# Performance work log

Hardware: AMD Instinct MI355X
Metric: run time of the kernel (lower is better)

The kernel has to match this reference:

```python
import jax, jax.numpy as jnp
import numpy as np

B, S, D = 32, 512, 512
H, DK, DV, DFF = 8, 64, 64, 2048
TEMP = float(np.sqrt(DK))  # d_k ** 0.5
COS_EPS = 1e-8             # torch.cosine_similarity eps
LN_EPS = 1e-5


def _layernorm(x, g, b):
    mu = jnp.mean(x, axis=-1, keepdims=True)
    var = jnp.var(x, axis=-1, keepdims=True)
    return (x - mu) * jax.lax.rsqrt(var + LN_EPS) * g + b


def setup_inputs() -> dict:
    key = jax.random.key(0)
    ks = jax.random.split(key, 12)
    s = 0.02
    return {
        "x": jax.random.normal(ks[0], (B, S, D), dtype=jnp.float32),
        "w_q": jax.random.normal(ks[1], (D, H * DK), dtype=jnp.float32) * s,
        "w_k": jax.random.normal(ks[2], (D, H * DK), dtype=jnp.float32) * s,
        "w_v": jax.random.normal(ks[3], (D, H * DV), dtype=jnp.float32) * s,
        "w_o": jax.random.normal(ks[4], (H * DV, D), dtype=jnp.float32) * s,
        "w_ff1": jax.random.normal(ks[5], (D, DFF), dtype=jnp.float32) * s,
        "b_ff1": jnp.zeros((DFF,), dtype=jnp.float32),
        "w_ff2": jax.random.normal(ks[6], (DFF, D), dtype=jnp.float32) * s,
        "b_ff2": jnp.zeros((D,), dtype=jnp.float32),
        "g1": jnp.ones((D,), dtype=jnp.float32),
        "b1": jnp.zeros((D,), dtype=jnp.float32),
        "g2": jnp.ones((D,), dtype=jnp.float32),
        "b2": jnp.zeros((D,), dtype=jnp.float32),
    }


def reference(x, w_q, w_k, w_v, w_o, w_ff1, b_ff1, w_ff2, b_ff2, g1, b1, g2, b2):
    b, s, _ = x.shape
    # projections -> [b, h, s, d]
    q = (x @ w_q).reshape(b, s, H, DK).transpose(0, 2, 1, 3)
    k = (x @ w_k).reshape(b, s, H, DK).transpose(0, 2, 1, 3)
    v = (x @ w_v).reshape(b, s, H, DV).transpose(0, 2, 1, 3)
    # cosine-similarity attention: dot(q,k) / max(||q||*||k||, eps) / temperature
    scores = jnp.einsum("bhqd,bhkd->bhqk", q, k)
    nq = jnp.linalg.norm(q, axis=-1)  # [b,h,s]
    nk = jnp.linalg.norm(k, axis=-1)
    denom = jnp.maximum(nq[:, :, :, None] * nk[:, :, None, :], COS_EPS)
    attn = jax.nn.softmax(scores / denom / TEMP, axis=-1)
    out = jnp.einsum("bhqk,bhkd->bhqd", attn, v)  # [b,h,s,dv]
    out = out.transpose(0, 2, 1, 3).reshape(b, s, H * DV) @ w_o
    # residual + LN1
    h1 = _layernorm(x + out, g1, b1)
    # FFN
    ffn = jax.nn.relu(h1 @ w_ff1 + b_ff1) @ w_ff2 + b_ff2
    # residual + LN2
    return _layernorm(h1 + ffn, g2, b2)
```

## Files before the change

kernel.cpp:

```cpp
#include <hip/hip_runtime.h>
#include <cmath>

typedef __bf16 bf16x8 __attribute__((ext_vector_type(8)));
typedef __bf16 bf16x4 __attribute__((ext_vector_type(4)));
typedef float  floatx4 __attribute__((ext_vector_type(4)));

#define LN_EPS 1e-5f
#define INV_TEMP 0.125f

static const int Mrows = 16384;

__device__ __forceinline__ void gload_lds16(const void* g, void* l) {
  __builtin_amdgcn_global_load_lds(
      (const __attribute__((address_space(1))) void*)g,
      (__attribute__((address_space(3))) void*)l, 16, 0, 0);
}

__global__ __launch_bounds__(256) void prep_kernel(const float* __restrict__ x, __bf16* __restrict__ xb,
                                                   const float* __restrict__ wq, const float* __restrict__ wk,
                                                   const float* __restrict__ wv, const float* __restrict__ wo,
                                                   const float* __restrict__ wff1, const float* __restrict__ wff2,
                                                   __bf16* __restrict__ tq, __bf16* __restrict__ tk,
                                                   __bf16* __restrict__ tv, __bf16* __restrict__ to_,
                                                   __bf16* __restrict__ tff1, __bf16* __restrict__ tff2) {
  const int bid = blockIdx.x, tid = threadIdx.x;
  if (bid < 8192) {
    int i = bid * 256 + tid;
    float4 v = ((const float4*)x)[i];
    __bf16* d = xb + i * 4;
    d[0] = (__bf16)v.x; d[1] = (__bf16)v.y; d[2] = (__bf16)v.z; d[3] = (__bf16)v.w;
    return;
  }
  __shared__ __bf16 til[64][72];
  int t = bid - 8192;
  const float* src; __bf16* dst; int R, C, bx, by;
  if (t < 256) {
    int w = t >> 6, tt = t & 63;
    const float* srcs[4] = {wq, wk, wv, wo};
    __bf16* dsts[4] = {tq, tk, tv, to_};
    src = srcs[w]; dst = dsts[w]; R = 512; C = 512; bx = tt & 7; by = tt >> 3;
  } else if (t < 512) {
    int tt = t - 256;
    src = wff1; dst = tff1; R = 512; C = 2048; bx = tt & 31; by = tt >> 5;
  } else {
    int tt = t - 512;
    src = wff2; dst = tff2; R = 2048; C = 512; bx = tt & 7; by = tt >> 3;
  }
  const float* s = src + (size_t)(by * 64) * C + bx * 64;
  int r = tid >> 4, c4 = (tid & 15) * 4;
  for (int p = 0; p < 4; ++p) {
    int rr = r + p * 16;
    float4 v = *(const float4*)(s + (size_t)rr * C + c4);
    til[c4 + 0][rr] = (__bf16)v.x;
    til[c4 + 1][rr] = (__bf16)v.y;
    til[c4 + 2][rr] = (__bf16)v.z;
    til[c4 + 3][rr] = (__bf16)v.w;
  }
  __syncthreads();
  __bf16* d = dst + (size_t)(bx * 64) * R + by * 64;
  int orow = tid >> 3, oc8 = (tid & 7) * 8;
  for (int p = 0; p < 2; ++p) {
    int rr = orow + p * 32;
    *(bf16x8*)(d + (size_t)rr * R + oc8) = *(const bf16x8*)(&til[rr][oc8]);
  }
}

template <int EPI, int NBN, int NDIM, int KDIM, int NKS>
__global__ __launch_bounds__(512, 4) void gemm256(const __bf16* __restrict__ A,
                                                  const __bf16* __restrict__ Bt,
                                                  __bf16* __restrict__ Cv,
                                                  const float* __restrict__ bias,
                                                  float* __restrict__ norms,
                                                  __bf16* __restrict__ vtg) {
  __shared__ __align__(16) char smem[73728];
  const int tid = threadIdx.x;
  const int wave = tid >> 6, lane = tid & 63;
  const int l15 = lane & 15, quad = lane >> 4;
  const int wm = wave >> 2, wn = wave & 3;

  constexpr int NBM = Mrows / 128;
  constexpr int NBLK = NBM * NBN * NKS;
  constexpr int KS = KDIM / NKS;
  constexpr int NTH = KS / 32;

  int id = blockIdx.x;
  int t = (id & 7) * (NBLK >> 3) + (id >> 3);
  const int ks = t / (NBM * NBN);
  t -= ks * (NBM * NBN);
  const int nblk = t % NBN, mblk = t / NBN;
  const int m0 = mblk * 128, n0 = nblk * 256;
  const __bf16* Ab = A + (size_t)ks * KS;
  const __bf16* Bb = Bt + (size_t)ks * KS;
  __bf16* Cw = Cv + (size_t)ks * Mrows * NDIM;
  (void)bias;

  const int l3 = lane >> 3, s_ = lane & 7;
  const int rl = l3 * 2 + (s_ >> 2);
  const int ksw = (s_ & 3) ^ (l3 & 3);
  const __bf16* sb[3];
  int ldo[3];
#pragma unroll
  for (int j = 0; j < 3; ++j) {
    int c = wave * 3 + j;
    int isB = c >= 8 ? 1 : 0;
    int cc = c - isB * 8;
    int row = cc * 16 + rl;
    sb[j] = (isB ? Bb + (size_t)(n0 + row) * KDIM
                 : Ab + (size_t)(m0 + row) * KDIM) + ksw * 8;
    ldo[j] = isB * 8192 + cc * 1024 + lane * 16;
  }

  const int lrt = (l15 >> 1) * 128 + (((l15 & 1) * 4 + (quad ^ ((l15 >> 1) & 3))) * 16);

  floatx4 zero = {0.f, 0.f, 0.f, 0.f};
  floatx4 acc[4][4];
#pragma unroll
  for (int i = 0; i < 4; ++i)
#pragma unroll
    for (int j = 0; j < 4; ++j) acc[i][j] = zero;

#define STAGEH(h, slotIdx)                                                   \
  {                                                                          \
    _Pragma("unroll") for (int j = 0; j < 3; ++j)                            \
        gload_lds16(sb[j] + (h) * 32, smem + (slotIdx) * 24576 + ldo[j]);    \
  }

#define READMFMA(slotIdx)                                                    \
  {                                                                          \
    const char* slotp = smem + (slotIdx) * 24576;                            \
    bf16x8 aF[4], bF[4];                                                     \
    _Pragma("unroll") for (int i = 0; i < 4; ++i)                            \
      aF[i] = *(const bf16x8*)(slotp + (wm * 4 + i) * 1024 + lrt);           \
    _Pragma("unroll") for (int j = 0; j < 4; ++j)                            \
      bF[j] = *(const bf16x8*)(slotp + 8192 + (wn * 4 + j) * 1024 + lrt);    \
    DOSTAGE_HOOK;                                                            \
    __builtin_amdgcn_s_setprio(1);                                           \
    _Pragma("unroll") for (int i = 0; i < 4; ++i)                            \
      _Pragma("unroll") for (int j = 0; j < 4; ++j)                          \
        acc[i][j] = __builtin_amdgcn_mfma_f32_16x16x32_bf16(aF[i], bF[j],    \
                                                            acc[i][j], 0, 0, 0); \
    __builtin_amdgcn_s_setprio(0);                                           \
  }

  STAGEH(0, 0);
  STAGEH(1, 1);

  int sl = 0;
  for (int h = 0; h < NTH - 1; ++h) {
    asm volatile("s_waitcnt vmcnt(3)" ::: "memory");
    __builtin_amdgcn_s_barrier();
    int st = (sl == 0) ? 2 : sl - 1;
    if (h < NTH - 2) {
#define DOSTAGE_HOOK STAGEH(h + 2, st)
      READMFMA(sl);
#undef DOSTAGE_HOOK
    } else {
#define DOSTAGE_HOOK
      READMFMA(sl);
#undef DOSTAGE_HOOK
    }
    sl = (sl == 2) ? 0 : sl + 1;
  }
  asm volatile("s_waitcnt vmcnt(0)" ::: "memory");
  __builtin_amdgcn_s_barrier();
#define DOSTAGE_HOOK
  READMFMA(sl);
#undef DOSTAGE_HOOK

#undef STAGEH
#undef READMFMA

  if (EPI == 4) {
    int head_global = (n0 + wn * 64) >> 6;
    int kind = head_global >> 3;
    if (kind < 2) {
      int h = head_global & 7;
#pragma unroll
      for (int ii = 0; ii < 4; ++ii)
#pragma unroll
        for (int r = 0; r < 4; ++r) {
          float sq = 0.f;
#pragma unroll
          for (int jj = 0; jj < 4; ++jj) {
            float v = acc[ii][jj][r];
            sq += v * v;
          }
          for (int m = 1; m < 16; m <<= 1) sq += __shfl_xor(sq, m, 64);
          if (l15 == 0) {
            int arow = m0 + wm * 64 + ii * 16 + quad * 4 + r;
            int bb = arow >> 9, ss = arow & 511;
            norms[kind * 131072 + ((bb << 3) + h) * 512 + ss] = rsqrtf(sq);
          }
        }
    } else {
      const int PADT = 72;
      __bf16* Ct = (__bf16*)smem;
      int bb = m0 >> 9, s0r = m0 & 511;
#pragma unroll
      for (int hh = 0; hh < 2; ++hh) {
        __builtin_amdgcn_s_barrier();
        if (wm == hh) {
#pragma unroll
          for (int ii = 0; ii < 4; ++ii)
#pragma unroll
            for (int jj = 0; jj < 4; ++jj) {
              bf16x4 pk;
#pragma unroll
              for (int r = 0; r < 4; ++r) pk[r] = (__bf16)acc[ii][jj][r];
              *(bf16x4*)(Ct + (wn * 64 + jj * 16 + l15) * PADT + ii * 16 + quad * 4) = pk;
            }
        }
        __builtin_amdgcn_s_barrier();
#pragma unroll
        for (int p = 0; p < 4; ++p) {
          int c = p * 64 + (tid >> 3);
          int s8 = (tid & 7) * 8;
          int h = ((n0 + c) >> 6) & 7, d = c & 63;
          *(bf16x8*)(vtg + ((size_t)(((bb << 3) + h) * 64 + d)) * 512 + s0r + hh * 64 + s8) =
              *(const bf16x8*)(Ct + c * PADT + s8);
        }
      }
      return;
    }
  }

  const int PADC = 264;
  __bf16* Cs = (__bf16*)smem;
  float bv[4];
  if (EPI == 2) {
#pragma unroll
    for (int j = 0; j < 4; ++j) bv[j] = bias[n0 + wn * 64 + j * 16 + l15];
  }
#pragma unroll
  for (int hh = 0; hh < 2; ++hh) {
    __builtin_amdgcn_s_barrier();
    if (wm == hh) {
#pragma unroll
      for (int i = 0; i < 4; ++i)
#pragma unroll
        for (int j = 0; j < 4; ++j)
#pragma unroll
          for (int r = 0; r < 4; ++r) {
            float v = acc[i][j][r];
            if (EPI == 2) {
              v += bv[j];
              v = v > 0.f ? v : 0.f;
            }
            Cs[(i * 16 + quad * 4 + r) * PADC + wn * 64 + j * 16 + l15] = (__bf16)v;
          }
    }
    __builtin_amdgcn_s_barrier();
#pragma unroll
    for (int p = 0; p < 4; ++p) {
      int rowl = p * 16 + (tid >> 5);
      int c8 = (tid & 31) * 8;
      *(bf16x8*)(Cw + (size_t)(m0 + hh * 64 + rowl) * NDIM + n0 + c8) =
          *(const bf16x8*)(Cs + rowl * PADC + c8);
    }
  }
}

__global__ __launch_bounds__(256) void attn_kernel(const __bf16* __restrict__ qkv,
                                                   const __bf16* __restrict__ vtg,
                                                   const float* __restrict__ norms,
                                                   __bf16* __restrict__ out) {
  __shared__ __align__(16) __bf16 KV[2][8192];
  __shared__ __align__(16) __bf16 P2[4][16 * 72];
  const int tid = threadIdx.x, wave = tid >> 6, lane = tid & 63;
  const int l15 = lane & 15, quad = lane >> 4;
  const int bh = blockIdx.x & 255;
  const int qq = blockIdx.x >> 8;
  const int b = bh >> 3, h = bh & 7;
  const int qbase = qq * 128 + wave * 32;
  const int rs = lane >> 3;
  const int swz_st = ((lane & 7) ^ rs) * 8;
  const int s7 = l15 & 7;

  const __bf16* Qb = qkv + (size_t)(b * 512) * 1536 + h * 64;
  const __bf16* Kb = Qb + 512;
  const __bf16* Vtb = vtg + (size_t)bh * 32768;
  const float* nkinv = norms + 131072 + bh * 512;
  const float* nqinv = norms + bh * 512;
  __bf16* Pw = P2[wave];

  bf16x8 aq[2][2];
  float cq[2];
  for (int ch = 0; ch < 2; ++ch) {
    int qrow = qbase + ch * 16;
    aq[ch][0] = *(const bf16x8*)(Qb + (size_t)(qrow + l15) * 1536 + quad * 8);
    aq[ch][1] = *(const bf16x8*)(Qb + (size_t)(qrow + l15) * 1536 + 32 + quad * 8);
    cq[ch] = nqinv[qrow + l15] * INV_TEMP;
  }

  floatx4 zero = {0.f, 0.f, 0.f, 0.f};
  floatx4 o[2][4];
  float lsum[2] = {0.f, 0.f};
  for (int ch = 0; ch < 2; ++ch)
    for (int jd = 0; jd < 4; ++jd) o[ch][jd] = zero;

#define STAGEKV(kt, s)                                                        \
  {                                                                           \
    int s0q = (kt) * 64;                                                      \
    _Pragma("unroll") for (int c = 0; c < 4; ++c) {                           \
      int g = wave * 4 + c;                                                   \
      const __bf16* src;                                                      \
      __bf16* dst;                                                            \
      if (g < 8) {                                                            \
        int sk = g * 8 + rs;                                                  \
        src = Kb + (size_t)(s0q + sk) * 1536 + swz_st;                        \
        dst = KV[s] + g * 512;                                                \
      } else {                                                                \
        int g2 = g - 8;                                                       \
        int dd = g2 * 8 + rs;                                                 \
        src = Vtb + (size_t)dd * 512 + s0q + swz_st;                          \
        dst = KV[s] + 4096 + g2 * 512;                                        \
      }                                                                       \
      gload_lds16(src, dst + lane * 8);                                       \
    }                                                                         \
  }

  STAGEKV(0, 0);

  for (int kt = 0; kt < 8; ++kt) {
    int s0 = kt * 64;
    int sl = kt & 1;
    asm volatile("s_waitcnt vmcnt(0)" ::: "memory");
    __builtin_amdgcn_s_barrier();
    if (kt < 7) STAGEKV(kt + 1, sl ^ 1);
    const __bf16* Ks = KV[sl];
    const __bf16* Vs = KV[sl] + 4096;

    floatx4 nk[4];
#pragma unroll
    for (int j = 0; j < 4; ++j)
      nk[j] = *(const floatx4*)(nkinv + s0 + j * 16 + quad * 4);

    bf16x8 kf[4][2];
#pragma unroll
    for (int j = 0; j < 4; ++j) {
      int r64 = (j * 16 + l15) * 64;
      kf[j][0] = *(const bf16x8*)(Ks + r64 + ((quad ^ s7) * 8));
      kf[j][1] = *(const bf16x8*)(Ks + r64 + (((4 + quad) ^ s7) * 8));
    }

    floatx4 z[2][4];
    __builtin_amdgcn_s_setprio(1);
#pragma unroll
    for (int ch = 0; ch < 2; ++ch)
#pragma unroll
      for (int j = 0; j < 4; ++j) {
        floatx4 zz = zero;
        zz = __builtin_amdgcn_mfma_f32_16x16x32_bf16(kf[j][0], aq[ch][0], zz, 0, 0, 0);
        zz = __builtin_amdgcn_mfma_f32_16x16x32_bf16(kf[j][1], aq[ch][1], zz, 0, 0, 0);
        z[ch][j] = zz;
      }
    __builtin_amdgcn_s_setprio(0);

    bf16x8 vf[4][2];
#pragma unroll
    for (int jd = 0; jd < 4; ++jd) {
      int r64 = (jd * 16 + l15) * 64;
      vf[jd][0] = *(const bf16x8*)(Vs + r64 + ((quad ^ s7) * 8));
      vf[jd][1] = *(const bf16x8*)(Vs + r64 + (((4 + quad) ^ s7) * 8));
    }

#pragma unroll
    for (int ch = 0; ch < 2; ++ch) {
#pragma unroll
      for (int j = 0; j < 4; ++j) {
        bf16x4 pk;
#pragma unroll
        for (int r = 0; r < 4; ++r) {
          float p = __expf(z[ch][j][r] * cq[ch] * nk[j][r]);
          lsum[ch] += p;
          pk[r] = (__bf16)p;
        }
        *(bf16x4*)(Pw + l15 * 72 + j * 16 + quad * 4) = pk;
      }
      bf16x8 ap0 = *(const bf16x8*)(Pw + l15 * 72 + quad * 8);
      bf16x8 ap1 = *(const bf16x8*)(Pw + l15 * 72 + 32 + quad * 8);
      __builtin_amdgcn_s_setprio(1);
#pragma unroll
      for (int jd = 0; jd < 4; ++jd) {
        o[ch][jd] = __builtin_amdgcn_mfma_f32_16x16x32_bf16(vf[jd][0], ap0, o[ch][jd], 0, 0, 0);
        o[ch][jd] = __builtin_amdgcn_mfma_f32_16x16x32_bf16(vf[jd][1], ap1, o[ch][jd], 0, 0, 0);
      }
      __builtin_amdgcn_s_setprio(0);
    }
  }
#undef STAGEKV

  for (int ch = 0; ch < 2; ++ch) {
    float s = lsum[ch];
    s += __shfl_xor(s, 16, 64);
    s += __shfl_xor(s, 32, 64);
    float inv = __builtin_amdgcn_rcpf(s);
    int q = qbase + ch * 16 + l15;
    __bf16* op = out + (size_t)(b * 512 + q) * 512 + h * 64;
    for (int jd = 0; jd < 4; ++jd) {
      bf16x4 pk;
      for (int r = 0; r < 4; ++r) pk[r] = (__bf16)(o[ch][jd][r] * inv);
      *(bf16x4*)(op + jd * 16 + quad * 4) = pk;
    }
  }
}

template <bool X1BF, bool WF, bool WB, bool DUAL>
__global__ __launch_bounds__(256) void resid_ln(const float* __restrict__ X1f,
                                                const __bf16* __restrict__ X1b,
                                                const __bf16* __restrict__ X2,
                                                const __bf16* __restrict__ X2b,
                                                const float* __restrict__ bias,
                                                const float* __restrict__ g,
                                                const float* __restrict__ be,
                                                float* __restrict__ outf,
                                                __bf16* __restrict__ outb) {
  int row = blockIdx.x * 4 + (threadIdx.x >> 6);
  int lane = threadIdx.x & 63;
  float v[8];
  bf16x8 b8 = *(const bf16x8*)(X2 + (size_t)row * 512 + lane * 8);
  if (X1BF) {
    bf16x8 a = *(const bf16x8*)(X1b + (size_t)row * 512 + lane * 8);
    for (int i = 0; i < 8; ++i) v[i] = (float)a[i] + (float)b8[i];
  } else {
    const float4* r1 = (const float4*)(X1f + (size_t)row * 512);
    float4 a0 = r1[lane * 2], a1 = r1[lane * 2 + 1];
    v[0] = a0.x; v[1] = a0.y; v[2] = a0.z; v[3] = a0.w;
    v[4] = a1.x; v[5] = a1.y; v[6] = a1.z; v[7] = a1.w;
    for (int i = 0; i < 8; ++i) v[i] += (float)b8[i];
  }
  if (DUAL) {
    bf16x8 c8 = *(const bf16x8*)(X2b + (size_t)row * 512 + lane * 8);
    for (int i = 0; i < 8; ++i) v[i] += (float)c8[i];
  }
  if (bias) {
    const float* bp = bias + lane * 8;
    for (int i = 0; i < 8; ++i) v[i] += bp[i];
  }
  float s = 0.f, sq = 0.f;
  for (int i = 0; i < 8; ++i) {
    s += v[i];
    sq += v[i] * v[i];
  }
  for (int m = 1; m < 64; m <<= 1) {
    s += __shfl_xor(s, m, 64);
    sq += __shfl_xor(sq, m, 64);
  }
  float mean = s * (1.f / 512.f);
  float var = sq * (1.f / 512.f) - mean * mean;
  float rstd = rsqrtf(var + LN_EPS);
  const float* gp = g + lane * 8;
  const float* bp2 = be + lane * 8;
  float o[8];
  for (int i = 0; i < 8; ++i) o[i] = (v[i] - mean) * rstd * gp[i] + bp2[i];
  if (WF) {
    float4 w0 = {o[0], o[1], o[2], o[3]}, w1 = {o[4], o[5], o[6], o[7]};
    ((float4*)(outf + (size_t)row * 512))[lane * 2] = w0;
    ((float4*)(outf + (size_t)row * 512))[lane * 2 + 1] = w1;
  }
  if (WB) {
    __bf16 tmp[8];
    for (int i = 0; i < 8; ++i) tmp[i] = (__bf16)o[i];
    *(bf16x8*)(outb + (size_t)row * 512 + lane * 8) = *(bf16x8*)tmp;
  }
}

extern "C" void kernel_launch(void* const* d_in, const int* in_sizes, int n_in,
                              void* d_out, int out_size, void* d_ws, size_t ws_size,
                              hipStream_t stream) {
  const float* x     = (const float*)d_in[0];
  const float* w_q   = (const float*)d_in[1];
  const float* w_k   = (const float*)d_in[2];
  const float* w_v   = (const float*)d_in[3];
  const float* w_o   = (const float*)d_in[4];
  const float* w_ff1 = (const float*)d_in[5];
  const float* b_ff1 = (const float*)d_in[6];
  const float* w_ff2 = (const float*)d_in[7];
  const float* b_ff2 = (const float*)d_in[8];
  const float* g1    = (const float*)d_in[9];
  const float* b1    = (const float*)d_in[10];
  const float* g2    = (const float*)d_in[11];
  const float* b2    = (const float*)d_in[12];
  float* out = (float*)d_out;

  char* ws = (char*)d_ws;
  size_t off = 0;
  auto alloc = [&](size_t bytes) -> void* {
    void* p = ws + off;
    off += (bytes + 255) & ~(size_t)255;
    return p;
  };
  __bf16* xb     = (__bf16*)alloc((size_t)Mrows * 512 * 2);
  __bf16* wt_qkv = (__bf16*)alloc((size_t)1536 * 512 * 2);
  __bf16* wt_o   = (__bf16*)alloc((size_t)512 * 512 * 2);
  __bf16* wt_ff1 = (__bf16*)alloc((size_t)2048 * 512 * 2);
  __bf16* wt_ff2 = (__bf16*)alloc((size_t)512 * 2048 * 2);
  __bf16* qkv    = (__bf16*)alloc((size_t)Mrows * 1536 * 2);
  float*  norms  = (float*)alloc((size_t)262144 * 4);
  __bf16* attn   = (__bf16*)alloc((size_t)Mrows * 512 * 2);
  __bf16* projb  = (__bf16*)alloc((size_t)Mrows * 512 * 2);
  __bf16* h1b    = (__bf16*)alloc((size_t)Mrows * 512 * 2);
  __bf16* mid    = (__bf16*)alloc((size_t)Mrows * 2048 * 2);
  __bf16* vtg    = mid;
  __bf16* wo_p   = mid;
  __bf16* f2o    = attn;

  prep_kernel<<<8960, 256, 0, stream>>>(x, xb, w_q, w_k, w_v, w_o, w_ff1, w_ff2,
                                        wt_qkv, wt_qkv + 512 * 512, wt_qkv + 2 * 512 * 512,
                                        wt_o, wt_ff1, wt_ff2);

  gemm256<4, 6, 1536, 512, 1><<<dim3(768), 512, 0, stream>>>(xb, wt_qkv, qkv, nullptr,
                                                             norms, vtg);
  attn_kernel<<<dim3(1024), 256, 0, stream>>>(qkv, vtg, norms, attn);
  gemm256<0, 2, 512, 512, 2><<<dim3(512), 512, 0, stream>>>(attn, wt_o, wo_p, nullptr,
                                                            nullptr, nullptr);
  resid_ln<false, false, true, true><<<4096, 256, 0, stream>>>(x, nullptr, wo_p,
                                                               wo_p + (size_t)Mrows * 512,
                                                               nullptr, g1, b1, nullptr, h1b);
  gemm256<2, 8, 2048, 512, 1><<<dim3(1024), 512, 0, stream>>>(h1b, wt_ff1, mid, b_ff1,
                                                              nullptr, nullptr);
  gemm256<0, 2, 512, 2048, 2><<<dim3(512), 512, 0, stream>>>(mid, wt_ff2, f2o, nullptr,
                                                             nullptr, nullptr);
  resid_ln<true, true, false, true><<<4096, 256, 0, stream>>>(nullptr, h1b, f2o,
                                                              f2o + (size_t)Mrows * 512,
                                                              b_ff2, g2, b2, out, nullptr);
}
```

Measured before the change: 307.3 us.

## Add 256x256-tile triple-buffered GEMM kernel for FFN1 projection

Introduces gemmBig, a GEMM with 256x256 output tiles per 512-thread block, a three-slot LDS ring, and global loads issued between the LDS fragment reads and the MFMA batch, with raised wave priority around the MFMAs. It replaces the previous gemm256 launch for the FFN first layer (bias+ReLU epilogue), halving the block count. The larger tile raises data reuse per LDS load and cuts global traffic. In exchange it uses 96KB of LDS and 128 accumulator floats per thread, which may limit occupancy.

```diff
diff --git a/kernel.cpp b/kernel.cpp
--- a/kernel.cpp
+++ b/kernel.cpp
@@ -255,6 +255,137 @@
       int rowl = p * 16 + (tid >> 5);
       int c8 = (tid & 31) * 8;
       *(bf16x8*)(Cw + (size_t)(m0 + hh * 64 + rowl) * NDIM + n0 + c8) =
+          *(const bf16x8*)(Cs + rowl * PADC + c8);
+    }
+  }
+}
+
+template <int EPI, int NBN, int NDIM, int KDIM>
+__global__ __launch_bounds__(512, 2) void gemmBig(const __bf16* __restrict__ A,
+                                                  const __bf16* __restrict__ Bt,
+                                                  __bf16* __restrict__ Cv,
+                                                  const float* __restrict__ bias) {
+  __shared__ __align__(16) char smem[98304];
+  const int tid = threadIdx.x;
+  const int wave = tid >> 6, lane = tid & 63;
+  const int l15 = lane & 15, quad = lane >> 4;
+  const int wm = wave >> 2, wn = wave & 3;
+
+  constexpr int NBM = Mrows / 256;
+  constexpr int NBLK = NBM * NBN;
+  constexpr int NTH = KDIM / 32;
+
+  int id = blockIdx.x;
+  int t = (id & 7) * (NBLK >> 3) + (id >> 3);
+  const int nblk = t % NBN, mblk = t / NBN;
+  const int m0 = mblk * 256, n0 = nblk * 256;
+
+  const int l3 = lane >> 3, s_ = lane & 7;
+  const int rl = l3 * 2 + (s_ >> 2);
+  const int ksw = (s_ & 3) ^ (l3 & 3);
+  const __bf16* sb[4];
+  int ldo[4];
+#pragma unroll
+  for (int j = 0; j < 4; ++j) {
+    int c = wave * 4 + j;
+    int isB = c >= 16 ? 1 : 0;
+    int row = (c - isB * 16) * 16 + rl;
+    sb[j] = (isB ? Bt + (size_t)(n0 + row) * KDIM
+                 : A + (size_t)(m0 + row) * KDIM) + ksw * 8;
+    ldo[j] = c * 1024 + lane * 16;
+  }
+
+  const int lrt = (l15 >> 1) * 128 + (((l15 & 1) * 4 + (quad ^ ((l15 >> 1) & 3))) * 16);
+
+  floatx4 zero = {0.f, 0.f, 0.f, 0.f};
+  floatx4 acc[8][4];
+#pragma unroll
+  for (int i = 0; i < 8; ++i)
+#pragma unroll
+    for (int j = 0; j < 4; ++j) acc[i][j] = zero;
+
+#define STAGEB(h, slotIdx)                                                   \
+  {                                                                          \
+    _Pragma("unroll") for (int j = 0; j < 4; ++j)                            \
+        gload_lds16(sb[j] + (h) * 32, smem + (slotIdx) * 32768 + ldo[j]);    \
+  }
+
+#define READMFMAB(slotIdx)                                                   \
+  {                                                                          \
+    const char* slotp = smem + (slotIdx) * 32768;                            \
+    bf16x8 aF[8], bF[4];                                                     \
+    _Pragma("unroll") for (int j = 0; j < 4; ++j)                            \
+      bF[j] = *(const bf16x8*)(slotp + 16384 + (wn * 4 + j) * 1024 + lrt);   \
+    _Pragma("unroll") for (int i = 0; i < 8; ++i)                            \
+      aF[i] = *(const bf16x8*)(slotp + (wm * 8 + i) * 1024 + lrt);           \
+    DOSTAGE_HOOK;                                                            \
+    __builtin_amdgcn_s_setprio(1);                                           \
+    _Pragma("unroll") for (int i = 0; i < 8; ++i)                            \
+      _Pragma("unroll") for (int j = 0; j < 4; ++j)                          \
+        acc[i][j] = __builtin_amdgcn_mfma_f32_16x16x32_bf16(aF[i], bF[j],    \
+                                                            acc[i][j], 0, 0, 0); \
+    __builtin_amdgcn_s_setprio(0);                                           \
+  }
+
+  STAGEB(0, 0);
+  STAGEB(1, 1);
+
+  int sl = 0;
+  for (int h = 0; h < NTH - 1; ++h) {
+    asm volatile("s_waitcnt vmcnt(4)" ::: "memory");
+    __builtin_amdgcn_s_barrier();
+    int st = (sl == 0) ? 2 : sl - 1;
+    if (h < NTH - 2) {
+#define DOSTAGE_HOOK STAGEB(h + 2, st)
+      READMFMAB(sl);
+#undef DOSTAGE_HOOK
+    } else {
+#define DOSTAGE_HOOK
+      READMFMAB(sl);
+#undef DOSTAGE_HOOK
+    }
+    sl = (sl == 2) ? 0 : sl + 1;
+  }
+  asm volatile("s_waitcnt vmcnt(0)" ::: "memory");
+  __builtin_amdgcn_s_barrier();
+#define DOSTAGE_HOOK
+  READMFMAB(sl);
+#undef DOSTAGE_HOOK
+
+#undef STAGEB
+#undef READMFMAB
+
+  const int PADC = 264;
+  __bf16* Cs = (__bf16*)smem;
+  float bv[4];
+  if (EPI == 2) {
+#pragma unroll
+    for (int j = 0; j < 4; ++j) bv[j] = bias[n0 + wn * 64 + j * 16 + l15];
+  }
+#pragma unroll
+  for (int hh = 0; hh < 2; ++hh) {
+    __builtin_amdgcn_s_barrier();
+    if (wm == hh) {
+#pragma unroll
+      for (int i = 0; i < 8; ++i)
+#pragma unroll
+        for (int j = 0; j < 4; ++j)
+#pragma unroll
+          for (int r = 0; r < 4; ++r) {
+            float v = acc[i][j][r];
+            if (EPI == 2) {
+              v += bv[j];
+              v = v > 0.f ? v : 0.f;
+            }
+            Cs[(i * 16 + quad * 4 + r) * PADC + wn * 64 + j * 16 + l15] = (__bf16)v;
+          }
+    }
+    __builtin_amdgcn_s_barrier();
+#pragma unroll
+    for (int p = 0; p < 8; ++p) {
+      int rowl = p * 16 + (tid >> 5);
+      int c8 = (tid & 31) * 8;
+      *(bf16x8*)(Cv + (size_t)(m0 + hh * 128 + rowl) * NDIM + n0 + c8) =
           *(const bf16x8*)(Cs + rowl * PADC + c8);
     }
   }
@@ -315,7 +446,7 @@
         src = Vtb + (size_t)dd * 512 + s0q + swz_st;                          \
         dst = KV[s] + 4096 + g2 * 512;                                        \
       }                                                                       \
-      gload_lds16(src, dst + lane * 8);                                       \
+      gload_lds16(src, dst + lane * 8);                                      \
     }                                                                         \
   }
 
@@ -517,8 +648,7 @@
   resid_ln<false, false, true, true><<<4096, 256, 0, stream>>>(x, nullptr, wo_p,
                                                                wo_p + (size_t)Mrows * 512,
                                                                nullptr, g1, b1, nullptr, h1b);
-  gemm256<2, 8, 2048, 512, 1><<<dim3(1024), 512, 0, stream>>>(h1b, wt_ff1, mid, b_ff1,
-                                                              nullptr, nullptr);
+  gemmBig<2, 8, 2048, 512><<<dim3(512), 512, 0, stream>>>(h1b, wt_ff1, mid, b_ff1);
   gemm256<0, 2, 512, 2048, 2><<<dim3(512), 512, 0, stream>>>(mid, wt_ff2, f2o, nullptr,
                                                              nullptr, nullptr);
   resid_ln<true, true, false, true><<<4096, 256, 0, stream>>>(nullptr, h1b, f2o,
```

Measured after the change: 299.0 us. 1.03x faster.

## Fuse output-projection and FFN2 GEMMs with residual-add LayerNorm epilogue

Applied to the files above, without the earlier changes.

Adds a gemmLN kernel that computes a 64x512 full-row output tile per block, so the residual add, bias and LayerNorm can run in the GEMM epilogue through a cross-wave shared-memory reduction. It replaces the split-K gemm256 plus separate resid_ln launches for both the attention output projection and FFN2. This removes the bf16 partial-sum round trips through global memory and two kernel launches. In exchange only 256 blocks launch, which limits parallelism, and the epilogue uses scalar, poorly coalesced loads and stores.

```diff
diff --git a/kernel.cpp b/kernel.cpp
--- a/kernel.cpp
+++ b/kernel.cpp
@@ -258,6 +258,181 @@
           *(const bf16x8*)(Cs + rowl * PADC + c8);
     }
   }
+}
+
+template <bool RESF32, bool OUTF32, bool HASB, int KDIM>
+__global__ __launch_bounds__(512, 2) void gemmLN(const __bf16* __restrict__ A,
+                                                 const __bf16* __restrict__ Bt,
+                                                 const float* __restrict__ resf,
+                                                 const __bf16* __restrict__ resb,
+                                                 const float* __restrict__ bias,
+                                                 const float* __restrict__ g,
+                                                 const float* __restrict__ be,
+                                                 float* __restrict__ outf,
+                                                 __bf16* __restrict__ outb) {
+  __shared__ __align__(16) char smem[110592];
+  const int tid = threadIdx.x;
+  const int wave = tid >> 6, lane = tid & 63;
+  const int l15 = lane & 15, quad = lane >> 4;
+
+  constexpr int NBLK = Mrows / 64;
+  constexpr int NTH = KDIM / 32;
+
+  int id = blockIdx.x;
+  int t = (id & 7) * (NBLK >> 3) + (id >> 3);
+  const int m0 = t * 64;
+
+  const int l3 = lane >> 3, s_ = lane & 7;
+  const int rl = l3 * 2 + (s_ >> 2);
+  const int ksw = (s_ & 3) ^ (l3 & 3);
+  const __bf16* sbB[4];
+  int ldoB[4];
+#pragma unroll
+  for (int j = 0; j < 4; ++j) {
+    int c = wave * 4 + j;
+    sbB[j] = Bt + (size_t)(c * 16 + rl) * KDIM + ksw * 8;
+    ldoB[j] = 4096 + c * 1024 + lane * 16;
+  }
+  const __bf16* sbA = A + (size_t)(m0 + wave * 16 + rl) * KDIM + ksw * 8;
+  const int ldoA = wave * 1024 + lane * 16;
+
+  const int lrt = (l15 >> 1) * 128 + (((l15 & 1) * 4 + (quad ^ ((l15 >> 1) & 3))) * 16);
+
+  floatx4 zero = {0.f, 0.f, 0.f, 0.f};
+  floatx4 acc[4][4];
+#pragma unroll
+  for (int i = 0; i < 4; ++i)
+#pragma unroll
+    for (int j = 0; j < 4; ++j) acc[i][j] = zero;
+
+#define STAGELN(h, slotIdx)                                                  \
+  {                                                                          \
+    _Pragma("unroll") for (int j = 0; j < 4; ++j)                            \
+        gload_lds16(sbB[j] + (h) * 32, smem + (slotIdx) * 36864 + ldoB[j]);  \
+    if (wave < 4)                                                            \
+      gload_lds16(sbA + (h) * 32, smem + (slotIdx) * 36864 + ldoA);          \
+  }
+
+#define VMWAITLN()                                                           \
+  {                                                                          \
+    if (wave < 4) asm volatile("s_waitcnt vmcnt(5)" ::: "memory");           \
+    else          asm volatile("s_waitcnt vmcnt(4)" ::: "memory");           \
+  }
+
+#define READMFMALN(slotIdx)                                                  \
+  {                                                                          \
+    const char* slotp = smem + (slotIdx) * 36864;                            \
+    bf16x8 aF[4], bF[4];                                                     \
+    _Pragma("unroll") for (int i = 0; i < 4; ++i)                            \
+      aF[i] = *(const bf16x8*)(slotp + i * 1024 + lrt);                      \
+    _Pragma("unroll") for (int j = 0; j < 4; ++j)                            \
+      bF[j] = *(const bf16x8*)(slotp + 4096 + (wave * 4 + j) * 1024 + lrt);  \
+    DOSTAGE_HOOK;                                                            \
+    __builtin_amdgcn_s_setprio(1);                                           \
+    _Pragma("unroll") for (int i = 0; i < 4; ++i)                            \
+      _Pragma("unroll") for (int j = 0; j < 4; ++j)                          \
+        acc[i][j] = __builtin_amdgcn_mfma_f32_16x16x32_bf16(aF[i], bF[j],    \
+                                                            acc[i][j], 0, 0, 0); \
+    __builtin_amdgcn_s_setprio(0);                                           \
+  }
+
+  STAGELN(0, 0);
+  STAGELN(1, 1);
+
+  int sl = 0;
+  for (int h = 0; h < NTH - 1; ++h) {
+    VMWAITLN();
+    __builtin_amdgcn_s_barrier();
+    int st = (sl == 0) ? 2 : sl - 1;
+    if (h < NTH - 2) {
+#define DOSTAGE_HOOK STAGELN(h + 2, st)
+      READMFMALN(sl);
+#undef DOSTAGE_HOOK
+    } else {
+#define DOSTAGE_HOOK
+      READMFMALN(sl);
+#undef DOSTAGE_HOOK
+    }
+    sl = (sl == 2) ? 0 : sl + 1;
+  }
+  asm volatile("s_waitcnt vmcnt(0)" ::: "memory");
+  __builtin_amdgcn_s_barrier();
+#define DOSTAGE_HOOK
+  READMFMALN(sl);
+#undef DOSTAGE_HOOK
+
+#undef STAGELN
+#undef VMWAITLN
+#undef READMFMALN
+
+  __syncthreads();
+  float* redS = (float*)smem;
+  float* redQ = (float*)(smem + 2048);
+  float* mstd = (float*)(smem + 4096);
+
+  float bv[4], gv[4], bev[4];
+#pragma unroll
+  for (int j = 0; j < 4; ++j) {
+    int col = wave * 64 + j * 16 + l15;
+    bv[j] = HASB ? bias[col] : 0.f;
+    gv[j] = g[col];
+    bev[j] = be[col];
+  }
+
+#pragma unroll
+  for (int i = 0; i < 4; ++i)
+#pragma unroll
+    for (int r = 0; r < 4; ++r) {
+      int rowl = i * 16 + quad * 4 + r;
+      size_t grow = (size_t)(m0 + rowl) * 512;
+      float s = 0.f, q = 0.f;
+#pragma unroll
+      for (int j = 0; j < 4; ++j) {
+        int col = wave * 64 + j * 16 + l15;
+        float rv = RESF32 ? resf[grow + col] : (float)resb[grow + col];
+        float v = acc[i][j][r] + bv[j] + rv;
+        acc[i][j][r] = v;
+        s += v;
+        q += v * v;
+      }
+      for (int m = 1; m < 16; m <<= 1) {
+        s += __shfl_xor(s, m, 64);
+        q += __shfl_xor(q, m, 64);
+      }
+      if (l15 == 0) {
+        redS[wave * 64 + rowl] = s;
+        redQ[wave * 64 + rowl] = q;
+      }
+    }
+  __syncthreads();
+  if (tid < 64) {
+    float s = 0.f, q = 0.f;
+#pragma unroll
+    for (int w = 0; w < 8; ++w) {
+      s += redS[w * 64 + tid];
+      q += redQ[w * 64 + tid];
+    }
+    float mean = s * (1.f / 512.f);
+    float var = q * (1.f / 512.f) - mean * mean;
+    mstd[tid] = mean;
+    mstd[64 + tid] = rsqrtf(var + LN_EPS);
+  }
+  __syncthreads();
+#pragma unroll
+  for (int i = 0; i < 4; ++i)
+#pragma unroll
+    for (int r = 0; r < 4; ++r) {
+      int rowl = i * 16 + quad * 4 + r;
+      size_t grow = (size_t)(m0 + rowl) * 512;
+      float mean = mstd[rowl], rstd = mstd[64 + rowl];
+#pragma unroll
+      for (int j = 0; j < 4; ++j) {
+        int col = wave * 64 + j * 16 + l15;
+        float o = (acc[i][j][r] - mean) * rstd * gv[j] + bev[j];
+        if (OUTF32) outf[grow + col] = o;
+        else        outb[grow + col] = (__bf16)o;
+      }
+    }
 }
 
 __global__ __launch_bounds__(256) void attn_kernel(const __bf16* __restrict__ qkv,
@@ -405,66 +580,6 @@
   }
 }
 
-template <bool X1BF, bool WF, bool WB, bool DUAL>
-__global__ __launch_bounds__(256) void resid_ln(const float* __restrict__ X1f,
-                                                const __bf16* __restrict__ X1b,
-                                                const __bf16* __restrict__ X2,
-                                                const __bf16* __restrict__ X2b,
-                                                const float* __restrict__ bias,
-                                                const float* __restrict__ g,
-                                                const float* __restrict__ be,
-                                                float* __restrict__ outf,
-                                                __bf16* __restrict__ outb) {
-  int row = blockIdx.x * 4 + (threadIdx.x >> 6);
-  int lane = threadIdx.x & 63;
-  float v[8];
-  bf16x8 b8 = *(const bf16x8*)(X2 + (size_t)row * 512 + lane * 8);
-  if (X1BF) {
-    bf16x8 a = *(const bf16x8*)(X1b + (size_t)row * 512 + lane * 8);
-    for (int i = 0; i < 8; ++i) v[i] = (float)a[i] + (float)b8[i];
-  } else {
-    const float4* r1 = (const float4*)(X1f + (size_t)row * 512);
-    float4 a0 = r1[lane * 2], a1 = r1[lane * 2 + 1];
-    v[0] = a0.x; v[1] = a0.y; v[2] = a0.z; v[3] = a0.w;
-    v[4] = a1.x; v[5] = a1.y; v[6] = a1.z; v[7] = a1.w;
-    for (int i = 0; i < 8; ++i) v[i] += (float)b8[i];
-  }
-  if (DUAL) {
-    bf16x8 c8 = *(const bf16x8*)(X2b + (size_t)row * 512 + lane * 8);
-    for (int i = 0; i < 8; ++i) v[i] += (float)c8[i];
-  }
-  if (bias) {
-    const float* bp = bias + lane * 8;
-    for (int i = 0; i < 8; ++i) v[i] += bp[i];
-  }
-  float s = 0.f, sq = 0.f;
-  for (int i = 0; i < 8; ++i) {
-    s += v[i];
-    sq += v[i] * v[i];
-  }
-  for (int m = 1; m < 64; m <<= 1) {
-    s += __shfl_xor(s, m, 64);
-    sq += __shfl_xor(sq, m, 64);
-  }
-  float mean = s * (1.f / 512.f);
-  float var = sq * (1.f / 512.f) - mean * mean;
-  float rstd = rsqrtf(var + LN_EPS);
-  const float* gp = g + lane * 8;
-  const float* bp2 = be + lane * 8;
-  float o[8];
-  for (int i = 0; i < 8; ++i) o[i] = (v[i] - mean) * rstd * gp[i] + bp2[i];
-  if (WF) {
-    float4 w0 = {o[0], o[1], o[2], o[3]}, w1 = {o[4], o[5], o[6], o[7]};
-    ((float4*)(outf + (size_t)row * 512))[lane * 2] = w0;
-    ((float4*)(outf + (size_t)row * 512))[lane * 2 + 1] = w1;
-  }
-  if (WB) {
-    __bf16 tmp[8];
-    for (int i = 0; i < 8; ++i) tmp[i] = (__bf16)o[i];
-    *(bf16x8*)(outb + (size_t)row * 512 + lane * 8) = *(bf16x8*)tmp;
-  }
-}
-
 extern "C" void kernel_launch(void* const* d_in, const int* in_sizes, int n_in,
                               void* d_out, int out_size, void* d_ws, size_t ws_size,
                               hipStream_t stream) {
@@ -498,12 +613,9 @@
   __bf16* qkv    = (__bf16*)alloc((size_t)Mrows * 1536 * 2);
   float*  norms  = (float*)alloc((size_t)262144 * 4);
   __bf16* attn   = (__bf16*)alloc((size_t)Mrows * 512 * 2);
-  __bf16* projb  = (__bf16*)alloc((size_t)Mrows * 512 * 2);
   __bf16* h1b    = (__bf16*)alloc((size_t)Mrows * 512 * 2);
   __bf16* mid    = (__bf16*)alloc((size_t)Mrows * 2048 * 2);
   __bf16* vtg    = mid;
-  __bf16* wo_p   = mid;
-  __bf16* f2o    = attn;
 
   prep_kernel<<<8960, 256, 0, stream>>>(x, xb, w_q, w_k, w_v, w_o, w_ff1, w_ff2,
                                         wt_qkv, wt_qkv + 512 * 512, wt_qkv + 2 * 512 * 512,
@@ -512,16 +624,12 @@
   gemm256<4, 6, 1536, 512, 1><<<dim3(768), 512, 0, stream>>>(xb, wt_qkv, qkv, nullptr,
                                                              norms, vtg);
   attn_kernel<<<dim3(1024), 256, 0, stream>>>(qkv, vtg, norms, attn);
-  gemm256<0, 2, 512, 512, 2><<<dim3(512), 512, 0, stream>>>(attn, wt_o, wo_p, nullptr,
-                                                            nullptr, nullptr);
-  resid_ln<false, false, true, true><<<4096, 256, 0, stream>>>(x, nullptr, wo_p,
-                                                               wo_p + (size_t)Mrows * 512,
-                                                               nullptr, g1, b1, nullptr, h1b);
+  gemmLN<true, false, false, 512><<<dim3(256), 512, 0, stream>>>(attn, wt_o, x, nullptr,
+                                                                 nullptr, g1, b1,
+                                                                 nullptr, h1b);
   gemm256<2, 8, 2048, 512, 1><<<dim3(1024), 512, 0, stream>>>(h1b, wt_ff1, mid, b_ff1,
                                                               nullptr, nullptr);
-  gemm256<0, 2, 512, 2048, 2><<<dim3(512), 512, 0, stream>>>(mid, wt_ff2, f2o, nullptr,
-                                                             nullptr, nullptr);
-  resid_ln<true, true, false, true><<<4096, 256, 0, stream>>>(nullptr, h1b, f2o,
-                                                              f2o + (size_t)Mrows * 512,
-                                                              b_ff2, g2, b2, out, nullptr);
+  gemmLN<false, true, true, 2048><<<dim3(256), 512, 0, stream>>>(mid, wt_ff2, nullptr, h1b,
+                                                                 b_ff2, g2, b2,
+                                                                 out, nullptr);
 }
```

New measurement: 304.5 us. Within noise of the previous version (-0.9%).
